# Kernel tuning notes

Hardware: AMD Instinct MI355X
Metric: run time of the kernel (lower is better)

Reference implementation:

```python
import jax, jax.numpy as jnp
import numpy as np

LRU_DIM = 256
HIDDEN = 256
H = 64
N = LRU_DIM // H  # 4 (even, per assert)
R_MIN, R_MAX, MAX_PHASE = 0.9, 0.999, 6.28
BSZ, T = 8, 4096


def _rotate_half(x):
    # interleaved pairs: [x0,x1,x2,x3,...] -> [-x1,x0,-x3,x2,...]
    r = jnp.stack([-x[..., 1::2], x[..., 0::2]], axis=-1)
    return r.reshape(x.shape)


def _mix_sequence(gamma, thetas, Us):
    # gamma: scalar, thetas: (N/2,), Us: (T,B,N) -> (T,B,N)
    Tlen = Us.shape[0]
    gammas = jnp.broadcast_to(gamma, (Tlen,))
    ths = jnp.broadcast_to(thetas, (Tlen,) + thetas.shape)

    def binf(a, b):
        gi, ti, xi = a
        gj, tj, xj = b
        theta = jnp.repeat(tj, 2, axis=-1)            # (T, N): [t0,t0,t1,t1,...]
        sin = jnp.sin(theta)[..., None, :]            # (T,1,N)
        cos = jnp.cos(theta)[..., None, :]
        acc = gj[..., None, None] * (cos * xi + sin * _rotate_half(xi)) + xj
        return (gi * gj, ti + tj, acc)

    _, _, res = jax.lax.associative_scan(binf, (gammas, ths, Us), axis=0)
    return res


def setup_inputs() -> dict:
    key = jax.random.key(0)
    ks = jax.random.split(key, 7)
    scale = 1.0 / np.sqrt(HIDDEN + LRU_DIM)
    u = jax.random.normal(ks[0], (BSZ, HIDDEN, T), dtype=jnp.float32)
    thetas_log = jnp.log(jax.random.uniform(ks[1], (H, N // 2), minval=0.01, maxval=1.0) * MAX_PHASE).astype(jnp.float32)
    P_param = (jax.random.normal(ks[2], (H, N, N), dtype=jnp.float32) / np.sqrt(LRU_DIM + N)).astype(jnp.float32)
    B_param = (jax.random.normal(ks[3], (H, N, HIDDEN), dtype=jnp.float32) * scale).astype(jnp.float32)
    C = (jax.random.normal(ks[4], (HIDDEN, LRU_DIM), dtype=jnp.float32) * scale).astype(jnp.float32)
    D = jax.random.normal(ks[5], (HIDDEN,), dtype=jnp.float32)
    u1 = jax.random.uniform(ks[6], (H,))
    gamma_log = (np.log(-np.log(R_MAX)) + u1 * (np.log(-np.log(R_MIN)) - np.log(-np.log(R_MAX)))).astype(jnp.float32)
    return {"u": u, "thetas_log": thetas_log, "P_param": P_param,
            "B_param": B_param, "C": C, "D": D, "gamma_log": gamma_log}


def reference(u, thetas_log, P_param, B_param, C, D, gamma_log):
    Bsz, hidden, Tlen = u.shape
    ut = jnp.transpose(u, (0, 2, 1))                       # (B,T,Dh)
    gamma = jnp.exp(-jnp.exp(gamma_log))                   # (H,)
    trace_per_head = jnp.sum(B_param * B_param, axis=(1, 2))  # tr(B B^T) per head
    norm = jnp.sqrt((1.0 - gamma ** 2) / trace_per_head)
    B_norm = norm[:, None, None] * B_param                 # (H,N,Dh)
    skew = P_param - jnp.swapaxes(P_param, 1, 2)
    P = jax.vmap(jax.scipy.linalg.expm)(skew)              # (H,N,N), orthogonal
    Us = jnp.einsum('HnD,BTD->HTBn', B_norm, ut)           # (H,T,B,N)
    Us = jnp.einsum('HNn,HTBn->HTBN', P, Us)               # == einsum with P^T as in torch
    thetas = jnp.exp(thetas_log)                           # (H,N/2)
    y = jax.vmap(_mix_sequence)(gamma, thetas, Us)         # (H,T,B,N)
    y = jnp.einsum('HNn,HTBN->HTBn', P, y)
    y = jnp.transpose(y, (2, 1, 0, 3)).reshape(Bsz, Tlen, -1)  # (B,T,lru_dim)
    y = jnp.einsum('Dn,BTn->BTD', C, y) + D * ut
    return jnp.transpose(y, (0, 2, 1))                     # (B,Dh,T)
```

## Files before the change

kernel.cpp:

```cpp
#include <hip/hip_runtime.h>
#include <math.h>


typedef __attribute__((ext_vector_type(8))) short short8;
typedef __attribute__((ext_vector_type(4))) float f32x4;

#define TLEN 4096
#define LCH 32
#define NCH 128
#define BSZ 8
#define LDW 132
#define LDK 264

constexpr int MB_OFF   = 0;
constexpr int CB_OFF   = 32768;
constexpr int AP_OFF   = 65536;
constexpr int ALP_OFF  = AP_OFF + (LCH + 1) * 256;
constexpr int TOT_OFF  = ALP_OFF + (NCH + 1) * 256;
constexpr int ZST_OFF  = TOT_OFF + NCH * BSZ * 256;

__device__ __forceinline__ float bfbits2f(unsigned int bits16) {
  union { unsigned int u; float f; } v; v.u = bits16 << 16; return v.f;
}
__device__ __forceinline__ unsigned int f2bfbits(float f) {
  union { float f; unsigned int u; } v; v.f = f;
  return (v.u + 0x7fffu + ((v.u >> 16) & 1u)) >> 16;
}
__device__ __forceinline__ unsigned int pack2(float x, float y) {
  return f2bfbits(x) | (f2bfbits(y) << 16);
}

__global__ __launch_bounds__(256) void k0_setup(
    const float* __restrict__ thetas_log, const float* __restrict__ P_param,
    const float* __restrict__ B_param, const float* __restrict__ C,
    const float* __restrict__ gamma_log, float* __restrict__ ws) {
  const int h = blockIdx.x;
  const int tid = threadIdx.x;
  __shared__ float red[4];
  __shared__ float Psh[16];
  __shared__ float nrmsh;

  {
    float4 v = *(const float4*)(B_param + (size_t)h * 1024 + tid * 4);
    float s = v.x * v.x + v.y * v.y + v.z * v.z + v.w * v.w;
#pragma unroll
    for (int off = 32; off > 0; off >>= 1) s += __shfl_down(s, off);
    if ((tid & 63) == 0) red[tid >> 6] = s;
  }
  __syncthreads();

  if (tid == 0) {
    double A[4][4], E[4][4], Tm[4][4];
    for (int i = 0; i < 4; ++i)
      for (int j = 0; j < 4; ++j)
        A[i][j] = (double)P_param[h * 16 + i * 4 + j] - (double)P_param[h * 16 + j * 4 + i];
    double fro = 0.0;
    for (int i = 0; i < 4; ++i) for (int j = 0; j < 4; ++j) fro += A[i][j] * A[i][j];
    fro = sqrt(fro);
    int s = 0;
    while (fro > 0.25 && s < 30) { fro *= 0.5; ++s; }
    double scl = 1.0;
    for (int q2 = 0; q2 < s; ++q2) scl *= 0.5;
    for (int i = 0; i < 4; ++i) for (int j = 0; j < 4; ++j) A[i][j] *= scl;
    for (int i = 0; i < 4; ++i)
      for (int j = 0; j < 4; ++j) { E[i][j] = (i == j) ? 1.0 : 0.0; Tm[i][j] = E[i][j]; }
    for (int k = 1; k <= 16; ++k) {
      double Tn[4][4];
      for (int i = 0; i < 4; ++i)
        for (int j = 0; j < 4; ++j) {
          double acc = 0.0;
          for (int m = 0; m < 4; ++m) acc += Tm[i][m] * A[m][j];
          Tn[i][j] = acc / (double)k;
        }
      for (int i = 0; i < 4; ++i)
        for (int j = 0; j < 4; ++j) { Tm[i][j] = Tn[i][j]; E[i][j] += Tn[i][j]; }
    }
    for (int q2 = 0; q2 < s; ++q2) {
      double E2[4][4];
      for (int i = 0; i < 4; ++i)
        for (int j = 0; j < 4; ++j) {
          double acc = 0.0;
          for (int m = 0; m < 4; ++m) acc += E[i][m] * E[m][j];
          E2[i][j] = acc;
        }
      for (int i = 0; i < 4; ++i) for (int j = 0; j < 4; ++j) E[i][j] = E2[i][j];
    }
    for (int i = 0; i < 4; ++i)
      for (int j = 0; j < 4; ++j) Psh[i * 4 + j] = (float)E[i][j];
  } else if (tid == 64 || tid == 65) {
    const int p = h * 2 + (tid - 64);
    double th = exp((double)thetas_log[p]);
    double g = exp(-exp((double)gamma_log[h]));
    double ar = g * cos(th), ai = g * sin(th);
    float2* Apw = (float2*)(ws + AP_OFF);
    double xr = 1.0, xi = 0.0;
    Apw[p] = make_float2(1.f, 0.f);
    for (int j = 1; j <= LCH; ++j) {
      double nr = xr * ar - xi * ai, ni = xr * ai + xi * ar;
      xr = nr; xi = ni;
      Apw[j * 128 + p] = make_float2((float)xr, (float)xi);
    }
  } else if (tid == 128) {
    double g = exp(-exp((double)gamma_log[h]));
    double tr = (double)red[0] + red[1] + red[2] + red[3];
    nrmsh = (float)sqrt((1.0 - g * g) / tr);
  }
  __syncthreads();

  unsigned short* Mbf = (unsigned short*)(ws + MB_OFF);
  unsigned int*   Cbd = (unsigned int*)(ws + CB_OFF);
  {
    float b0 = B_param[(h * 4 + 0) * 256 + tid];
    float b1 = B_param[(h * 4 + 1) * 256 + tid];
    float b2 = B_param[(h * 4 + 2) * 256 + tid];
    float b3 = B_param[(h * 4 + 3) * 256 + tid];
    float nrm = nrmsh;
#pragma unroll
    for (int N = 0; N < 4; ++N) {
      float acc = Psh[N * 4 + 0] * b0 + Psh[N * 4 + 1] * b1 +
                  Psh[N * 4 + 2] * b2 + Psh[N * 4 + 3] * b3;
      Mbf[(h * 4 + N) * 256 + tid] = (unsigned short)f2bfbits(nrm * acc);
    }
  }
  {
    float4 cv = *(const float4*)(C + (size_t)tid * 256 + h * 4);
    float o[4];
#pragma unroll
    for (int N = 0; N < 4; ++N)
      o[N] = cv.x * Psh[N * 4 + 0] + cv.y * Psh[N * 4 + 1] +
             cv.z * Psh[N * 4 + 2] + cv.w * Psh[N * 4 + 3];
    Cbd[(tid * 256 + h * 4) >> 1]       = pack2(o[0], o[1]);
    Cbd[((tid * 256 + h * 4) >> 1) + 1] = pack2(o[2], o[3]);
  }
}

__global__ __launch_bounds__(256, 4) void k1_mfma(
    const float* __restrict__ u, float* __restrict__ ws) {
  __shared__ __align__(16) unsigned char smem[LCH * LDK * 2];
  unsigned short* us = (unsigned short*)smem;
  unsigned int*   wd = (unsigned int*)smem;

  const int c = blockIdx.x, b = blockIdx.y;
  const int t0 = c * LCH;
  const int tid = threadIdx.x;
  const int L = tid & 63;
  const int w = __builtin_amdgcn_readfirstlane(tid >> 6);
  const int qh = L >> 4, l15 = L & 15;

  {
    const int dp = tid >> 3;
    const int t4 = (tid & 7) * 4;
#pragma unroll
    for (int i = 0; i < 4; ++i) {
      int j = dp + 32 * i;
      float4 va = *(const float4*)(u + (size_t)(b * 256 + 2 * j) * TLEN + t0 + t4);
      float4 vb = *(const float4*)(u + (size_t)(b * 256 + 2 * j + 1) * TLEN + t0 + t4);
      float av[4] = {va.x, va.y, va.z, va.w};
      float bv[4] = {vb.x, vb.y, vb.z, vb.w};
#pragma unroll
      for (int dt = 0; dt < 4; ++dt)
        wd[(t4 + dt) * LDW + j] = pack2(av[dt], bv[dt]);
    }
  }
  __syncthreads();

  f32x4 acc[4][2];
#pragma unroll
  for (int rt = 0; rt < 4; ++rt)
#pragma unroll
    for (int tt = 0; tt < 2; ++tt) acc[rt][tt] = (f32x4){0.f, 0.f, 0.f, 0.f};
  {
    const unsigned short* Mbf = (const unsigned short*)(ws + MB_OFF);
#pragma unroll
    for (int ks = 0; ks < 8; ++ks) {
      short8 af[4], bf[2];
#pragma unroll
      for (int rt = 0; rt < 4; ++rt)
        af[rt] = *(const short8*)(Mbf + (size_t)(w * 64 + rt * 16 + l15) * 256 + ks * 32 + qh * 8);
#pragma unroll
      for (int tt = 0; tt < 2; ++tt)
        bf[tt] = *(const short8*)(us + (tt * 16 + l15) * LDK + ks * 32 + qh * 8);
#pragma unroll
      for (int rt = 0; rt < 4; ++rt)
#pragma unroll
        for (int tt = 0; tt < 2; ++tt)
          acc[rt][tt] = __builtin_amdgcn_mfma_f32_16x16x32_bf16(af[rt], bf[tt], acc[rt][tt], 0, 0, 0);
    }
  }
  __syncthreads();

#pragma unroll
  for (int rt = 0; rt < 4; ++rt) {
    int pbase = w * 32 + rt * 8 + qh * 2;
#pragma unroll
    for (int tt = 0; tt < 2; ++tt) {
      int t = tt * 16 + l15;
      f32x4 a4 = acc[rt][tt];
      wd[t * LDW + pbase]     = pack2(a4[0], a4[1]);
      wd[t * LDW + pbase + 1] = pack2(a4[2], a4[3]);
    }
  }
  __syncthreads();

  if (tid < 128) {
    const int p = tid;
    const float2* Apw = (const float2*)(ws + AP_OFF);
    unsigned int* Zg = (unsigned int*)(ws + ZST_OFF) + (size_t)(c * BSZ + b) * 4096;
    float2 a = Apw[128 + p];
    float zr = 0.f, zi = 0.f;
#pragma unroll
    for (int t = 0; t < LCH; ++t) {
      unsigned int wv = wd[t * LDW + p];
      float wr = bfbits2f(wv & 0xffffu), wi = bfbits2f(wv >> 16);
      float nr = fmaf(a.x, zr, fmaf(-a.y, zi, wr));
      float ni = fmaf(a.x, zi, fmaf(a.y, zr, wi));
      zr = nr; zi = ni;
      Zg[t * 128 + p] = pack2(zr, zi);
    }
    ((float2*)(ws + TOT_OFF))[(c * BSZ + b) * 128 + p] = make_float2(zr, zi);
  }
}

__global__ __launch_bounds__(128) void k2_carry(float* __restrict__ ws) {
  const int b = blockIdx.x;
  const int p = threadIdx.x;
  const float2* Apw = (const float2*)(ws + AP_OFF);
  float2* Tot = (float2*)(ws + TOT_OFF);
  const float2 aL = Apw[LCH * 128 + p];
  float cr = 0.f, ci = 0.f;
  for (int c0 = 0; c0 < NCH; c0 += 16) {
    float2 tv[16];
#pragma unroll
    for (int k = 0; k < 16; ++k)
      tv[k] = Tot[(size_t)((c0 + k) * BSZ + b) * 128 + p];
#pragma unroll
    for (int k = 0; k < 16; ++k) {
      Tot[(size_t)((c0 + k) * BSZ + b) * 128 + p] = make_float2(cr, ci);
      float nr = fmaf(aL.x, cr, fmaf(-aL.y, ci, tv[k].x));
      float ni = fmaf(aL.x, ci, fmaf(aL.y, cr, tv[k].y));
      cr = nr; ci = ni;
    }
  }
}

__global__ __launch_bounds__(256, 4) void k3_mfma(
    const float* __restrict__ u, const float* __restrict__ Dv,
    const float* __restrict__ ws, float* __restrict__ out) {
  __shared__ __align__(16) unsigned char smem[LCH * LDK * 2];
  unsigned int* wd = (unsigned int*)smem;

  const int c = blockIdx.x, b = blockIdx.y;
  const int t0 = c * LCH;
  const int tid = threadIdx.x;
  const int L = tid & 63;
  const int w = __builtin_amdgcn_readfirstlane(tid >> 6);
  const int qh = L >> 4, l15 = L & 15;

  {
    const int p = tid & 127;
    const float2 cv = ((const float2*)(ws + TOT_OFF))[(size_t)(c * BSZ + b) * 128 + p];
    const float2* Apw = (const float2*)(ws + AP_OFF);
    const unsigned int* Zg = (const unsigned int*)(ws + ZST_OFF) + (size_t)(c * BSZ + b) * 4096;
#pragma unroll
    for (int jj = 0; jj < 16; ++jj) {
      int idx = tid + 256 * jj;
      int t = idx >> 7;
      unsigned int wv = Zg[idx];
      float2 ap = Apw[(t + 1) * 128 + p];
      float sr = fmaf(ap.x, cv.x, fmaf(-ap.y, cv.y, bfbits2f(wv & 0xffffu)));
      float si = fmaf(ap.x, cv.y, fmaf(ap.y, cv.x, bfbits2f(wv >> 16)));
      wd[t * LDW + p] = pack2(sr, si);
    }
  }
  __syncthreads();

  f32x4 acc[4][2];
#pragma unroll
  for (int rt = 0; rt < 4; ++rt)
#pragma unroll
    for (int tt = 0; tt < 2; ++tt) acc[rt][tt] = (f32x4){0.f, 0.f, 0.f, 0.f};
  {
    const unsigned short* Cbf = (const unsigned short*)(ws + CB_OFF);
    const unsigned short* zs  = (const unsigned short*)smem;
#pragma unroll
    for (int ks = 0; ks < 8; ++ks) {
      short8 af[4], bf[2];
#pragma unroll
      for (int rt = 0; rt < 4; ++rt)
        af[rt] = *(const short8*)(Cbf + (size_t)(w * 64 + rt * 16 + l15) * 256 + ks * 32 + qh * 8);
#pragma unroll
      for (int tt = 0; tt < 2; ++tt)
        bf[tt] = *(const short8*)(zs + (tt * 16 + l15) * LDK + ks * 32 + qh * 8);
#pragma unroll
      for (int rt = 0; rt < 4; ++rt)
#pragma unroll
        for (int tt = 0; tt < 2; ++tt)
          acc[rt][tt] = __builtin_amdgcn_mfma_f32_16x16x32_bf16(af[rt], bf[tt], acc[rt][tt], 0, 0, 0);
    }
  }

  float dv[4][4];
#pragma unroll
  for (int rt = 0; rt < 4; ++rt)
#pragma unroll
    for (int q = 0; q < 4; ++q) dv[rt][q] = Dv[w * 64 + rt * 16 + qh * 4 + q];
#pragma unroll
  for (int rt = 0; rt < 4; ++rt) {
    int Dbase = w * 64 + rt * 16 + qh * 4;
#pragma unroll
    for (int tt = 0; tt < 2; ++tt) {
      int t = tt * 16 + l15;
      f32x4 a4 = acc[rt][tt];
      size_t obase = (size_t)(b * 256 + Dbase) * TLEN + t0 + t;
#pragma unroll
      for (int q = 0; q < 4; ++q)
        out[obase + (size_t)q * TLEN] = a4[q] + dv[rt][q] * u[obase + (size_t)q * TLEN];
    }
  }
}

extern "C" void kernel_launch(void* const* d_in, const int* in_sizes, int n_in,
                              void* d_out, int out_size, void* d_ws, size_t ws_size,
                              hipStream_t stream) {
  const float* u          = (const float*)d_in[0];
  const float* thetas_log = (const float*)d_in[1];
  const float* P_param    = (const float*)d_in[2];
  const float* B_param    = (const float*)d_in[3];
  const float* C          = (const float*)d_in[4];
  const float* Dvec       = (const float*)d_in[5];
  const float* gamma_log  = (const float*)d_in[6];
  float* out = (float*)d_out;
  float* ws  = (float*)d_ws;

  hipLaunchKernelGGL(k0_setup, dim3(64), dim3(256), 0, stream,
                     thetas_log, P_param, B_param, C, gamma_log, ws);
  hipLaunchKernelGGL(k1_mfma, dim3(NCH, BSZ), dim3(256), 0, stream, u, ws);
  hipLaunchKernelGGL(k2_carry, dim3(BSZ), dim3(128), 0, stream, ws);
  hipLaunchKernelGGL(k3_mfma, dim3(NCH, BSZ), dim3(256), 0, stream, u, Dvec, ws, out);
}
```

Measured before the change: 157.4 us.

## Fuse carry scan into k1 via last-block atomic counter, add nontemporal accesses

```diff
diff --git a/kernel.cpp b/kernel.cpp
--- a/kernel.cpp
+++ b/kernel.cpp
@@ -15,8 +15,8 @@
 constexpr int MB_OFF   = 0;
 constexpr int CB_OFF   = 32768;
 constexpr int AP_OFF   = 65536;
-constexpr int ALP_OFF  = AP_OFF + (LCH + 1) * 256;
-constexpr int TOT_OFF  = ALP_OFF + (NCH + 1) * 256;
+constexpr int CNT_OFF  = AP_OFF + (LCH + 1) * 256;
+constexpr int TOT_OFF  = CNT_OFF + (NCH + 1) * 256;
 constexpr int ZST_OFF  = TOT_OFF + NCH * BSZ * 256;
 
 __device__ __forceinline__ float bfbits2f(unsigned int bits16) {
@@ -39,6 +39,8 @@
   __shared__ float red[4];
   __shared__ float Psh[16];
   __shared__ float nrmsh;
+
+  if (h == 0 && tid < BSZ) ((unsigned int*)(ws + CNT_OFF))[tid] = 0u;
 
   {
     float4 v = *(const float4*)(B_param + (size_t)h * 1024 + tid * 4);
@@ -136,9 +138,9 @@
 
 __global__ __launch_bounds__(256, 4) void k1_mfma(
     const float* __restrict__ u, float* __restrict__ ws) {
-  __shared__ __align__(16) unsigned char smem[LCH * LDK * 2];
-  unsigned short* us = (unsigned short*)smem;
-  unsigned int*   wd = (unsigned int*)smem;
+  __shared__ __align__(16) unsigned short us[LCH * LDK];
+  __shared__ __align__(16) unsigned int   wd[LCH * LDW];
+  __shared__ unsigned int lastsh;
 
   const int c = blockIdx.x, b = blockIdx.y;
   const int t0 = c * LCH;
@@ -148,18 +150,19 @@
   const int qh = L >> 4, l15 = L & 15;
 
   {
+    unsigned int* usd = (unsigned int*)us;
     const int dp = tid >> 3;
     const int t4 = (tid & 7) * 4;
 #pragma unroll
     for (int i = 0; i < 4; ++i) {
       int j = dp + 32 * i;
-      float4 va = *(const float4*)(u + (size_t)(b * 256 + 2 * j) * TLEN + t0 + t4);
-      float4 vb = *(const float4*)(u + (size_t)(b * 256 + 2 * j + 1) * TLEN + t0 + t4);
-      float av[4] = {va.x, va.y, va.z, va.w};
-      float bv[4] = {vb.x, vb.y, vb.z, vb.w};
+      f32x4 va = __builtin_nontemporal_load(
+          (const f32x4*)(u + (size_t)(b * 256 + 2 * j) * TLEN + t0 + t4));
+      f32x4 vb = __builtin_nontemporal_load(
+          (const f32x4*)(u + (size_t)(b * 256 + 2 * j + 1) * TLEN + t0 + t4));
 #pragma unroll
       for (int dt = 0; dt < 4; ++dt)
-        wd[(t4 + dt) * LDW + j] = pack2(av[dt], bv[dt]);
+        usd[(t4 + dt) * LDW + j] = pack2(va[dt], vb[dt]);
     }
   }
   __syncthreads();
@@ -187,7 +190,6 @@
           acc[rt][tt] = __builtin_amdgcn_mfma_f32_16x16x32_bf16(af[rt], bf[tt], acc[rt][tt], 0, 0, 0);
     }
   }
-  __syncthreads();
 
 #pragma unroll
   for (int rt = 0; rt < 4; ++rt) {
@@ -219,26 +221,34 @@
     }
     ((float2*)(ws + TOT_OFF))[(c * BSZ + b) * 128 + p] = make_float2(zr, zi);
   }
-}
-
-__global__ __launch_bounds__(128) void k2_carry(float* __restrict__ ws) {
-  const int b = blockIdx.x;
-  const int p = threadIdx.x;
-  const float2* Apw = (const float2*)(ws + AP_OFF);
-  float2* Tot = (float2*)(ws + TOT_OFF);
-  const float2 aL = Apw[LCH * 128 + p];
-  float cr = 0.f, ci = 0.f;
-  for (int c0 = 0; c0 < NCH; c0 += 16) {
-    float2 tv[16];
-#pragma unroll
-    for (int k = 0; k < 16; ++k)
-      tv[k] = Tot[(size_t)((c0 + k) * BSZ + b) * 128 + p];
-#pragma unroll
-    for (int k = 0; k < 16; ++k) {
-      Tot[(size_t)((c0 + k) * BSZ + b) * 128 + p] = make_float2(cr, ci);
-      float nr = fmaf(aL.x, cr, fmaf(-aL.y, ci, tv[k].x));
-      float ni = fmaf(aL.x, ci, fmaf(aL.y, cr, tv[k].y));
-      cr = nr; ci = ni;
+  __syncthreads();
+
+  if (tid == 0) {
+    __threadfence();
+    unsigned int prev = __hip_atomic_fetch_add(
+        (unsigned int*)(ws + CNT_OFF) + b, 1u,
+        __ATOMIC_ACQ_REL, __HIP_MEMORY_SCOPE_AGENT);
+    lastsh = (prev == NCH - 1) ? 1u : 0u;
+  }
+  __syncthreads();
+  if (lastsh && tid < 128) {
+    const int p = tid;
+    const float2* Apw = (const float2*)(ws + AP_OFF);
+    float2* Tot = (float2*)(ws + TOT_OFF);
+    const float2 aL = Apw[LCH * 128 + p];
+    float cr = 0.f, ci = 0.f;
+    for (int c0 = 0; c0 < NCH; c0 += 16) {
+      float2 tv[16];
+#pragma unroll
+      for (int k = 0; k < 16; ++k)
+        tv[k] = Tot[(size_t)((c0 + k) * BSZ + b) * 128 + p];
+#pragma unroll
+      for (int k = 0; k < 16; ++k) {
+        Tot[(size_t)((c0 + k) * BSZ + b) * 128 + p] = make_float2(cr, ci);
+        float nr = fmaf(aL.x, cr, fmaf(-aL.y, ci, tv[k].x));
+        float ni = fmaf(aL.x, ci, fmaf(aL.y, cr, tv[k].y));
+        cr = nr; ci = ni;
+      }
     }
   }
 }
@@ -313,8 +323,11 @@
       f32x4 a4 = acc[rt][tt];
       size_t obase = (size_t)(b * 256 + Dbase) * TLEN + t0 + t;
 #pragma unroll
-      for (int q = 0; q < 4; ++q)
-        out[obase + (size_t)q * TLEN] = a4[q] + dv[rt][q] * u[obase + (size_t)q * TLEN];
+      for (int q = 0; q < 4; ++q) {
+        float uv = __builtin_nontemporal_load(u + obase + (size_t)q * TLEN);
+        __builtin_nontemporal_store(a4[q] + dv[rt][q] * uv,
+                                    out + obase + (size_t)q * TLEN);
+      }
     }
   }
 }
@@ -335,6 +348,5 @@
   hipLaunchKernelGGL(k0_setup, dim3(64), dim3(256), 0, stream,
                      thetas_log, P_param, B_param, C, gamma_log, ws);
   hipLaunchKernelGGL(k1_mfma, dim3(NCH, BSZ), dim3(256), 0, stream, u, ws);
-  hipLaunchKernelGGL(k2_carry, dim3(BSZ), dim3(128), 0, stream, ws);
   hipLaunchKernelGGL(k3_mfma, dim3(NCH, BSZ), dim3(256), 0, stream, u, Dvec, ws, out);
 }
```

Measured after the change: 225.6 us. +43.3%, slower.
